# Performance work log

Measured on AMD Instinct MI355X. Metric: run time of the kernel, lower is better.

The kernel has to match this reference:

```python
import jax, jax.numpy as jnp
import numpy as np
from jax import lax

B, CIN, COUT, H, W = 4, 256, 256, 64, 64
KH = KW = 3
STRIDE = PAD = DIL = 1
GROUPS = 1
K = KH * KW
HO = (H + 2 * PAD - DIL * (KH - 1) - 1) // STRIDE + 1
WO = (W + 2 * PAD - DIL * (KW - 1) - 1) // STRIDE + 1
DN = ('NCHW', 'OIHW', 'NCHW')


def _sep_conv(x, dw, pw):
    # Separable2d: depthwise kxk conv (stride/pad/dilation) then pointwise 1x1.
    y = lax.conv_general_dilated(x, dw, (STRIDE, STRIDE), [(PAD, PAD), (PAD, PAD)],
                                 rhs_dilation=(DIL, DIL), feature_group_count=x.shape[1],
                                 dimension_numbers=DN)
    return lax.conv_general_dilated(y, pw, (1, 1), 'VALID', dimension_numbers=DN)


def _deform_conv2d(x, offset, mask, weight, bias):
    Bb, Cin, Hh, Ww = x.shape
    O = weight.shape[0]
    G = offset.shape[1] // (2 * K)  # offset groups
    offs = offset.reshape(Bb, G, K, 2, HO, WO)
    dy, dx = offs[:, :, :, 0], offs[:, :, :, 1]  # [B,G,K,Ho,Wo]
    ki, kj = jnp.meshgrid(jnp.arange(KH), jnp.arange(KW), indexing='ij')
    base_y = (-PAD + ki.reshape(K, 1) * DIL + jnp.arange(HO)[None, :] * STRIDE).astype(x.dtype)  # [K,Ho]
    base_x = (-PAD + kj.reshape(K, 1) * DIL + jnp.arange(WO)[None, :] * STRIDE).astype(x.dtype)  # [K,Wo]
    py = base_y[None, None, :, :, None] + dy  # [B,G,K,Ho,Wo]
    px = base_x[None, None, :, None, :] + dx

    xg = x.reshape(Bb, G, Cin // G, Hh, Ww)

    def bilinear(img, py, px):
        # img [C,H,W], py/px [K,Ho,Wo]; zero-padding outside bounds.
        y0 = jnp.floor(py)
        x0 = jnp.floor(px)
        out = jnp.zeros((img.shape[0],) + py.shape, img.dtype)
        for a, (iy, wy) in enumerate((((y0), (y0 + 1 - py)), ((y0 + 1), (py - y0)))):
            for b, (ix, wx) in enumerate((((x0), (x0 + 1 - px)), ((x0 + 1), (px - x0)))):
                valid = (iy >= 0) & (iy < Hh) & (ix >= 0) & (ix < Ww)
                iyc = jnp.clip(iy, 0, Hh - 1).astype(jnp.int32)
                ixc = jnp.clip(ix, 0, Ww - 1).astype(jnp.int32)
                v = img[:, iyc, ixc]  # [C,K,Ho,Wo]
                out = out + v * (wy * wx * valid)[None]
        return out

    sampled = jax.vmap(jax.vmap(bilinear))(xg, py, px)  # [B,G,C/G,K,Ho,Wo]
    m = mask.reshape(Bb, G, K, HO, WO)
    sampled = sampled * m[:, :, None]

    cols = sampled.reshape(Bb, Cin, K, HO, WO).reshape(Bb, GROUPS, Cin // GROUPS, K, HO, WO)
    wr = weight.reshape(GROUPS, O // GROUPS, Cin // GROUPS, K)
    out = jnp.einsum('bgckhw,gock->bgohw', cols, wr).reshape(Bb, O, HO, WO)
    return out + bias[None, :, None, None]


def setup_inputs() -> dict:
    key = jax.random.key(0)
    ks = jax.random.split(key, 7)
    x = jax.random.normal(ks[0], (B, CIN, H, W), jnp.float32)
    weight = jax.random.normal(ks[1], (COUT, CIN // GROUPS, KH, KW), jnp.float32) / np.sqrt(CIN * K)
    bias = jax.random.normal(ks[2], (COUT,), jnp.float32) * 0.01
    off_dw = jax.random.normal(ks[3], (CIN, 1, KH, KW), jnp.float32) * 0.01
    off_pw = jax.random.normal(ks[4], (2 * K * GROUPS, CIN, 1, 1), jnp.float32) * 0.01
    mask_dw = jax.random.normal(ks[5], (CIN, 1, KH, KW), jnp.float32) * 0.01
    mask_pw = jax.random.normal(ks[6], (K * GROUPS, CIN, 1, 1), jnp.float32) * 0.01
    return dict(x=x, weight=weight, bias=bias, off_dw=off_dw, off_pw=off_pw,
                mask_dw=mask_dw, mask_pw=mask_pw)


def reference(x, weight, bias, off_dw, off_pw, mask_dw, mask_pw):
    offset = _sep_conv(x, off_dw, off_pw)                       # [B,2*K,Ho,Wo]
    mask = jax.nn.sigmoid(_sep_conv(x, mask_dw, mask_pw)) * 2.0  # MaskSigmoid(scale=2)
    return _deform_conv2d(x, offset, mask, weight, bias)
```

## Files before the change

### kernel.cpp

```cpp
#include <hip/hip_runtime.h>

#define CIN   256
#define COUT  256
#define HH    64
#define WW    64
#define KD    2304
#define NPIX  16384
#define SPLIT 16
#define CPS   (CIN / SPLIT)
#define NSTEP 18

typedef __attribute__((ext_vector_type(4))) float  float4v;
typedef __attribute__((ext_vector_type(4))) unsigned int uint4v;
typedef _Float16 h2 __attribute__((ext_vector_type(2)));
typedef _Float16 h8 __attribute__((ext_vector_type(8)));
typedef unsigned int u32;
typedef unsigned short u16;

__device__ __forceinline__ h2 as_h2(u32 v) { union { u32 u; h2 h; } x; x.u = v; return x.h; }
__device__ __forceinline__ u32 as_u32(h2 h) { union { u32 u; h2 h; } x; x.h = h; return x.u; }
__device__ __forceinline__ u16 f2h_bits(float f) { _Float16 h = (_Float16)f; return *(u16*)&h; }
__device__ __forceinline__ u32 packh2(float a, float b) {
  h2 h; h[0] = (_Float16)a; h[1] = (_Float16)b; return as_u32(h);
}

__device__ __forceinline__ void gload_lds16(const void* g, void* l) {
  __builtin_amdgcn_global_load_lds((const __attribute__((address_space(1))) u32*)g,
                                   (__attribute__((address_space(3))) u32*)l, 16, 0, 0);
}

__global__ __launch_bounds__(256) void offmask_part_kernel(
    const float* __restrict__ x,
    const float* __restrict__ off_dw, const float* __restrict__ off_pw,
    const float* __restrict__ mask_dw, const float* __restrict__ mask_pw,
    u32* __restrict__ part2, u16* __restrict__ xt)
{
  int m = blockIdx.x * 256 + threadIdx.x;
  int s = blockIdx.y;
  int b = m >> 12, pix = m & 4095;
  int ho = pix >> 6, wo = pix & 63;
  const float* xb = x + (size_t)b * CIN * 4096;

  float acc[27];
#pragma unroll
  for (int j = 0; j < 27; ++j) acc[j] = 0.f;
  u16 ctr[16];

  int c0 = s * CPS;
  for (int ci = 0; ci < CPS; ++ci) {
    int c = c0 + ci;
    const float* xc = xb + (size_t)c * 4096;
    float d_off = 0.f, d_msk = 0.f;
#pragma unroll
    for (int t = 0; t < 9; ++t) {
      int gy = ho + t / 3 - 1, gx = wo + t % 3 - 1;
      bool ok = (gy >= 0) & (gy < HH) & (gx >= 0) & (gx < WW);
      float v = ok ? xc[gy * 64 + gx] : 0.f;
      if (t == 4) ctr[ci] = f2h_bits(v);
      d_off += v * off_dw[c * 9 + t];
      d_msk += v * mask_dw[c * 9 + t];
    }
#pragma unroll
    for (int j = 0; j < 18; ++j) acc[j] += d_off * off_pw[j * 256 + c];
#pragma unroll
    for (int j = 0; j < 9; ++j) acc[18 + j] += d_msk * mask_pw[j * 256 + c];
  }
  *(uint4v*)(xt + (size_t)m * 256 + c0)     = *(uint4v*)&ctr[0];
  *(uint4v*)(xt + (size_t)m * 256 + c0 + 8) = *(uint4v*)&ctr[8];

  uint4v o[4];
#pragma unroll
  for (int k = 0; k < 13; ++k) o[k >> 2][k & 3] = packh2(acc[2 * k], acc[2 * k + 1]);
  o[3][1] = packh2(acc[26], 0.f);
  o[3][2] = 0; o[3][3] = 0;
  uint4v* pp = (uint4v*)(part2 + ((size_t)s * NPIX + m) * 16);
#pragma unroll
  for (int q = 0; q < 4; ++q) pp[q] = o[q];
}

__global__ __launch_bounds__(256) void offmask_reduce_kernel(
    const u32* __restrict__ part2, float* __restrict__ rec)
{
  int i = blockIdx.x * 256 + threadIdx.x;
  int m = i >> 4, k = i & 15;
  int j0 = 2 * k, j1 = 2 * k + 1;
  if (j0 >= 27) { rec[(size_t)m * 32 + j0] = 0.f; rec[(size_t)m * 32 + j1] = 0.f; return; }
  float s0 = 0.f, s1 = 0.f;
#pragma unroll
  for (int s = 0; s < SPLIT; ++s) {
    h2 v = as_h2(part2[((size_t)s * NPIX + m) * 16 + k]);
    s0 += (float)v[0]; s1 += (float)v[1];
  }
  rec[(size_t)m * 32 + j0] = (j0 < 18) ? s0 : 2.f / (1.f + __expf(-s0));
  rec[(size_t)m * 32 + j1] = (j1 < 18) ? s1 : ((j1 < 27) ? 2.f / (1.f + __expf(-s1)) : 0.f);
}

__global__ __launch_bounds__(256) void wconv_kernel(const float* __restrict__ w,
                                                    u16* __restrict__ wb)
{
  int i = blockIdx.x * 256 + threadIdx.x;
  int co = i / KD, rem = i - co * KD;
  int c = rem / 9, kk = rem - c * 9;
  wb[co * KD + kk * 256 + c] = f2h_bits(w[i]);
}

__global__ __launch_bounds__(512, 2) void gemm_fused_kernel(
    const u16* __restrict__ A,
    const u16* __restrict__ xt,
    const float* __restrict__ rec,
    u16* __restrict__ tmp4)
{
  __shared__ __align__(16) u16 lA[3][256 * 32];
  __shared__ __align__(16) u16 lB[2][256 * 32];
  const int tid = threadIdx.x;
  const int ord = blockIdx.x;
  const int xcd = ord & 7, slot = ord >> 3;
  const int ptile = (slot >> 2) * 8 + xcd;
  const int h     = slot & 3;
  const int m0  = ptile * 256;
  const int b_img = ptile >> 4;
  const int cbase = h * 64;
  const int wave = tid >> 6, lane = tid & 63;
  const int wm = wave >> 1, wn = wave & 1;
  const int rl = lane & 15, kq = lane >> 4;
  const int sA = (kq ^ (rl & 3) ^ ((rl >> 2) & 3)) * 8;

  const int rA  = tid >> 2;
  const int koA = ((tid & 3) ^ (rA & 3) ^ ((rA >> 2) & 3)) * 8;
  const u16* aRow0 = A + (size_t)rA * KD + koA;
  const u16* aRow1 = A + (size_t)(rA + 128) * KD + koA;

  const int px_t = tid >> 1;
  const int chh  = (tid & 1) * 16;
  const int m_px = m0 + px_t;
  const int ho = (m_px & 4095) >> 6, wo = m_px & 63;
  const float* rp = rec + (size_t)m_px * 32;
  const u16* xb = xt + (size_t)b_img * 4096 * 256;
  const int swzp = (px_t & 3) ^ ((px_t >> 2) & 3);
  const int wAddr0 = px_t * 32 + ((((tid & 1) * 2)     ^ swzp) * 8);
  const int wAddr1 = px_t * 32 + ((((tid & 1) * 2 + 1) ^ swzp) * 8);

  u32 cOff[4];
  h2  wh[4];

#define KCOL(t_) (((t_) >> 1) * 256 + cbase + ((t_) & 1) * 32)

#define CALC_CORNERS(kk_) do {                                             \
    float dy = rp[(kk_) * 2], dx = rp[(kk_) * 2 + 1], msk = rp[18 + (kk_)];\
    float py  = (float)(ho - 1 + ((kk_) / 3)) + dy;                        \
    float pxf = (float)(wo - 1 + ((kk_) % 3)) + dx;                        \
    float fy = floorf(py), fx = floorf(pxf);                               \
    int y0 = (int)fy, x0 = (int)fx;                                        \
    float wy1 = py - fy, wy0 = 1.f - wy1;                                  \
    float wx1 = pxf - fx, wx0 = 1.f - wx1;                                 \
    _Pragma("unroll")                                                      \
    for (int cr = 0; cr < 4; ++cr) {                                       \
      int iy = y0 + (cr >> 1), ix = x0 + (cr & 1);                         \
      bool valid = (iy >= 0) & (iy < HH) & (ix >= 0) & (ix < WW);          \
      int iyc = min(max(iy, 0), HH - 1), ixc = min(max(ix, 0), WW - 1);    \
      cOff[cr] = (u32)(iyc * 64 + ixc) * 256;                              \
      float wy = (cr >> 1) ? wy1 : wy0;                                    \
      float wx = (cr & 1) ? wx1 : wx0;                                     \
      float wf = valid ? (wy * wx * msk) : 0.f;                            \
      _Float16 hw = (_Float16)wf;                                          \
      wh[cr] = (h2){hw, hw};                                               \
    }                                                                      \
  } while (0)

#define STAGE_A(k_, slot_) do {                                            \
    int k0_ = KCOL(k_);                                                    \
    gload_lds16(aRow0 + k0_, lA[slot_] + tid * 8);                         \
    gload_lds16(aRow1 + k0_, lA[slot_] + (tid + 512) * 8);                 \
  } while (0)

#define SAMP_LOAD(t_, va, vb) do {                                         \
    int c0n_ = cbase + ((t_) & 1) * 32 + chh;                              \
    _Pragma("unroll")                                                      \
    for (int cr = 0; cr < 4; ++cr) {                                       \
      va[cr] = *(const uint4v*)(xb + cOff[cr] + c0n_);                     \
      vb[cr] = *(const uint4v*)(xb + cOff[cr] + c0n_ + 8);                 \
    }                                                                      \
  } while (0)

#define BLEND_WRITE(bufi_, va, vb) do {                                    \
    uint4v o0, o1;                                                         \
    _Pragma("unroll")                                                      \
    for (int w_ = 0; w_ < 4; ++w_) {                                       \
      h2 s0_ = wh[0] * as_h2(va[0][w_]) + wh[1] * as_h2(va[1][w_]);        \
      s0_   += wh[2] * as_h2(va[2][w_]) + wh[3] * as_h2(va[3][w_]);        \
      h2 s1_ = wh[0] * as_h2(vb[0][w_]) + wh[1] * as_h2(vb[1][w_]);        \
      s1_   += wh[2] * as_h2(vb[2][w_]) + wh[3] * as_h2(vb[3][w_]);        \
      o0[w_] = as_u32(s0_); o1[w_] = as_u32(s1_);                          \
    }                                                                      \
    *(uint4v*)&lB[bufi_][wAddr0] = o0;                                     \
    *(uint4v*)&lB[bufi_][wAddr1] = o1;                                     \
  } while (0)

  float4v acc[4][8];
#pragma unroll
  for (int m = 0; m < 4; ++m)
#pragma unroll
    for (int n = 0; n < 8; ++n) acc[m][n] = float4v{0.f, 0.f, 0.f, 0.f};

  {
    CALC_CORNERS(0);
    uint4v va[4], vb[4];
    SAMP_LOAD(0, va, vb);
    STAGE_A(0, 0);
    STAGE_A(1, 1);
    asm volatile("s_waitcnt vmcnt(2)" ::: "memory");
    BLEND_WRITE(0, va, vb);
    asm volatile("s_waitcnt lgkmcnt(0)" ::: "memory");
    __builtin_amdgcn_s_barrier();
  }

  for (int it = 0; it < 3; ++it) {
#pragma unroll
    for (int u = 0; u < 6; ++u) {
      const int t = it * 6 + u;
      const int tn  = (t + 1 == NSTEP) ? 0 : t + 1;
      const int tn2 = (t + 2 >= NSTEP) ? (t + 2 - NSTEP) : t + 2;
      if ((tn & 1) == 0) CALC_CORNERS(tn >> 1);
      uint4v va[4], vb[4];
      SAMP_LOAD(tn, va, vb);
      STAGE_A(tn2, (u + 2) % 3);
      h8 af[4], bf[8];
#pragma unroll
      for (int m = 0; m < 4; ++m)
        af[m] = *(const h8*)&lA[u % 3][(wm * 64 + m * 16 + rl) * 32 + sA];
#pragma unroll
      for (int n = 0; n < 8; ++n)
        bf[n] = *(const h8*)&lB[u & 1][(wn * 128 + n * 16 + rl) * 32 + sA];
#pragma unroll
      for (int m = 0; m < 4; ++m)
#pragma unroll
        for (int n = 0; n < 8; ++n)
          acc[m][n] = __builtin_amdgcn_mfma_f32_16x16x32_f16(af[m], bf[n], acc[m][n], 0, 0, 0);
      asm volatile("s_waitcnt vmcnt(2)" ::: "memory");
      BLEND_WRITE((u + 1) & 1, va, vb);
      asm volatile("s_waitcnt lgkmcnt(0)" ::: "memory");
      __builtin_amdgcn_s_barrier();
    }
  }
#undef STAGE_A
#undef CALC_CORNERS
#undef SAMP_LOAD
#undef BLEND_WRITE
#undef KCOL

  const int p_base = (m0 & 4095) + wn * 128;
  u16* db = tmp4 + (size_t)h * COUT * NPIX + (size_t)b_img * COUT * 4096;
#pragma unroll
  for (int m = 0; m < 4; ++m) {
#pragma unroll
    for (int j = 0; j < 4; ++j) {
      int co = wm * 64 + m * 16 + kq * 4 + j;
#pragma unroll
      for (int n = 0; n < 8; ++n) {
        int pp = p_base + n * 16 + rl;
        db[(size_t)co * 4096 + pp] = f2h_bits(acc[m][n][j]);
      }
    }
  }
}

__global__ __launch_bounds__(256) void add_kernel(const u16* __restrict__ tmp4,
                                                  const float* __restrict__ bias,
                                                  float* __restrict__ out)
{
  size_t i = ((size_t)blockIdx.x * 256 + threadIdx.x) * 8;
  int co = (int)((i >> 12) & 255);
  float bv = bias[co];
  uint4v v0 = *(const uint4v*)(tmp4 + i);
  uint4v v1 = *(const uint4v*)(tmp4 + (size_t)COUT * NPIX + i);
  uint4v v2 = *(const uint4v*)(tmp4 + (size_t)2 * COUT * NPIX + i);
  uint4v v3 = *(const uint4v*)(tmp4 + (size_t)3 * COUT * NPIX + i);
  float4v oA, oB;
#pragma unroll
  for (int w = 0; w < 4; ++w) {
    h2 a = as_h2(v0[w]), b = as_h2(v1[w]), c = as_h2(v2[w]), d = as_h2(v3[w]);
    float lo = (float)a[0] + (float)b[0] + (float)c[0] + (float)d[0] + bv;
    float hi = (float)a[1] + (float)b[1] + (float)c[1] + (float)d[1] + bv;
    if (w < 2) { oA[w * 2] = lo; oA[w * 2 + 1] = hi; }
    else       { oB[(w - 2) * 2] = lo; oB[(w - 2) * 2 + 1] = hi; }
  }
  *(float4v*)(out + i) = oA;
  *(float4v*)(out + i + 4) = oB;
}

extern "C" void kernel_launch(void* const* d_in, const int* in_sizes, int n_in,
                              void* d_out, int out_size, void* d_ws, size_t ws_size,
                              hipStream_t stream) {
  const float* x       = (const float*)d_in[0];
  const float* weight  = (const float*)d_in[1];
  const float* bias    = (const float*)d_in[2];
  const float* off_dw  = (const float*)d_in[3];
  const float* off_pw  = (const float*)d_in[4];
  const float* mask_dw = (const float*)d_in[5];
  const float* mask_pw = (const float*)d_in[6];

  if (ws_size < 45219840ull) return;
  float* rec   = (float*)d_ws;
  u16*   wb    = (u16*)((char*)d_ws + 2097152);
  u16*   xt    = (u16*)((char*)d_ws + 3276800);
  u32*   part2 = (u32*)((char*)d_ws + 11665408);
  u16*   tmp4  = (u16*)((char*)d_ws + 11665408);
  float* out   = (float*)d_out;

  wconv_kernel<<<dim3(2304), dim3(256), 0, stream>>>(weight, wb);
  offmask_part_kernel<<<dim3(NPIX / 256, SPLIT), dim3(256), 0, stream>>>(
      x, off_dw, off_pw, mask_dw, mask_pw, part2, xt);
  offmask_reduce_kernel<<<dim3(NPIX * 16 / 256), dim3(256), 0, stream>>>(part2, rec);
  gemm_fused_kernel<<<dim3(256), dim3(512), 0, stream>>>(wb, xt, rec, tmp4);
  add_kernel<<<dim3(COUT * NPIX / 8 / 256), dim3(256), 0, stream>>>(tmp4, bias, out);
}
```

Measured before the change: 93.79 us.

## Drop split-K in fused deform GEMM, keep sampled B in registers, fuse bias epilogue

The GEMM no longer splits the channel dimension four ways across blocks. Each block now owns 64 pixels across the full K=2304 and all 256 output channels, so the fp16 partial buffer and the separate add kernel go away and bias is added in the epilogue. Each wave samples its own 16 pixels straight into the MFMA B-operand registers, which removes the LDS B buffer and its write/barrier traffic. In exchange the weight matrix is streamed through LDS once per 64-pixel tile instead of once per 256-pixel tile (four times more A traffic). The launch also drops to 256-thread blocks with 72 smaller K steps, which means more barriers and less MFMA work per step.

```diff
diff --git a/kernel.cpp b/kernel.cpp
--- a/kernel.cpp
+++ b/kernel.cpp
@@ -8,7 +8,7 @@
 #define NPIX  16384
 #define SPLIT 16
 #define CPS   (CIN / SPLIT)
-#define NSTEP 18
+#define NSTEP 72
 
 typedef __attribute__((ext_vector_type(4))) float  float4v;
 typedef __attribute__((ext_vector_type(4))) unsigned int uint4v;
@@ -104,46 +104,38 @@
   wb[co * KD + kk * 256 + c] = f2h_bits(w[i]);
 }
 
-__global__ __launch_bounds__(512, 2) void gemm_fused_kernel(
+__global__ __launch_bounds__(256) void gemm_fused_kernel(
     const u16* __restrict__ A,
     const u16* __restrict__ xt,
     const float* __restrict__ rec,
-    u16* __restrict__ tmp4)
+    const float* __restrict__ bias,
+    float* __restrict__ out)
 {
   __shared__ __align__(16) u16 lA[3][256 * 32];
-  __shared__ __align__(16) u16 lB[2][256 * 32];
   const int tid = threadIdx.x;
-  const int ord = blockIdx.x;
-  const int xcd = ord & 7, slot = ord >> 3;
-  const int ptile = (slot >> 2) * 8 + xcd;
-  const int h     = slot & 3;
-  const int m0  = ptile * 256;
-  const int b_img = ptile >> 4;
-  const int cbase = h * 64;
+  const int ptile = blockIdx.x;
+  const int m0 = ptile * 64;
+  const int b_img = ptile >> 6;
   const int wave = tid >> 6, lane = tid & 63;
-  const int wm = wave >> 1, wn = wave & 1;
   const int rl = lane & 15, kq = lane >> 4;
   const int sA = (kq ^ (rl & 3) ^ ((rl >> 2) & 3)) * 8;
 
   const int rA  = tid >> 2;
   const int koA = ((tid & 3) ^ (rA & 3) ^ ((rA >> 2) & 3)) * 8;
-  const u16* aRow0 = A + (size_t)rA * KD + koA;
-  const u16* aRow1 = A + (size_t)(rA + 128) * KD + koA;
-
-  const int px_t = tid >> 1;
-  const int chh  = (tid & 1) * 16;
-  const int m_px = m0 + px_t;
+  const u16* aRow[4];
+#pragma unroll
+  for (int q = 0; q < 4; ++q) aRow[q] = A + (size_t)(rA + q * 64) * KD + koA;
+
+  const int m_px = m0 + wave * 16 + rl;
   const int ho = (m_px & 4095) >> 6, wo = m_px & 63;
   const float* rp = rec + (size_t)m_px * 32;
   const u16* xb = xt + (size_t)b_img * 4096 * 256;
-  const int swzp = (px_t & 3) ^ ((px_t >> 2) & 3);
-  const int wAddr0 = px_t * 32 + ((((tid & 1) * 2)     ^ swzp) * 8);
-  const int wAddr1 = px_t * 32 + ((((tid & 1) * 2 + 1) ^ swzp) * 8);
 
   u32 cOff[4];
   h2  wh[4];
-
-#define KCOL(t_) (((t_) >> 1) * 256 + cbase + ((t_) & 1) * 32)
+  uint4v sv[4];
+
+#define KCOL(t_) (((t_) >> 3) * 256 + ((t_) & 7) * 32)
 
 #define CALC_CORNERS(kk_) do {                                             \
     float dy = rp[(kk_) * 2], dx = rp[(kk_) * 2 + 1], msk = rp[18 + (kk_)];\
@@ -167,125 +159,86 @@
     }                                                                      \
   } while (0)
 
-#define STAGE_A(k_, slot_) do {                                            \
+#define STAGE_A(k_, sl_) do {                                              \
     int k0_ = KCOL(k_);                                                    \
-    gload_lds16(aRow0 + k0_, lA[slot_] + tid * 8);                         \
-    gload_lds16(aRow1 + k0_, lA[slot_] + (tid + 512) * 8);                 \
-  } while (0)
-
-#define SAMP_LOAD(t_, va, vb) do {                                         \
-    int c0n_ = cbase + ((t_) & 1) * 32 + chh;                              \
-    _Pragma("unroll")                                                      \
-    for (int cr = 0; cr < 4; ++cr) {                                       \
-      va[cr] = *(const uint4v*)(xb + cOff[cr] + c0n_);                     \
-      vb[cr] = *(const uint4v*)(xb + cOff[cr] + c0n_ + 8);                 \
+    _Pragma("unroll")                                                      \
+    for (int q = 0; q < 4; ++q)                                            \
+      gload_lds16(aRow[q] + k0_, lA[sl_] + q * 2048 + tid * 8);            \
+  } while (0)
+
+#define SAMP(t_) do {                                                      \
+    int c0_ = ((t_) & 7) * 32 + kq * 8;                                    \
+    _Pragma("unroll")                                                      \
+    for (int cr = 0; cr < 4; ++cr)                                         \
+      sv[cr] = *(const uint4v*)(xb + cOff[cr] + c0_);                      \
+  } while (0)
+
+#define BLEND(bf_) do {                                                    \
+    _Pragma("unroll")                                                      \
+    for (int w_ = 0; w_ < 4; ++w_) {                                       \
+      h2 s_ = wh[0] * as_h2(sv[0][w_]) + wh[1] * as_h2(sv[1][w_]);         \
+      s_   += wh[2] * as_h2(sv[2][w_]) + wh[3] * as_h2(sv[3][w_]);         \
+      ((u32*)&(bf_))[w_] = as_u32(s_);                                     \
     }                                                                      \
   } while (0)
 
-#define BLEND_WRITE(bufi_, va, vb) do {                                    \
-    uint4v o0, o1;                                                         \
-    _Pragma("unroll")                                                      \
-    for (int w_ = 0; w_ < 4; ++w_) {                                       \
-      h2 s0_ = wh[0] * as_h2(va[0][w_]) + wh[1] * as_h2(va[1][w_]);        \
-      s0_   += wh[2] * as_h2(va[2][w_]) + wh[3] * as_h2(va[3][w_]);        \
-      h2 s1_ = wh[0] * as_h2(vb[0][w_]) + wh[1] * as_h2(vb[1][w_]);        \
-      s1_   += wh[2] * as_h2(vb[2][w_]) + wh[3] * as_h2(vb[3][w_]);        \
-      o0[w_] = as_u32(s0_); o1[w_] = as_u32(s1_);                          \
-    }                                                                      \
-    *(uint4v*)&lB[bufi_][wAddr0] = o0;                                     \
-    *(uint4v*)&lB[bufi_][wAddr1] = o1;                                     \
-  } while (0)
-
-  float4v acc[4][8];
-#pragma unroll
-  for (int m = 0; m < 4; ++m)
-#pragma unroll
-    for (int n = 0; n < 8; ++n) acc[m][n] = float4v{0.f, 0.f, 0.f, 0.f};
+  float4v acc[16];
+#pragma unroll
+  for (int m = 0; m < 16; ++m) acc[m] = float4v{0.f, 0.f, 0.f, 0.f};
 
   {
     CALC_CORNERS(0);
-    uint4v va[4], vb[4];
-    SAMP_LOAD(0, va, vb);
+    SAMP(0);
     STAGE_A(0, 0);
     STAGE_A(1, 1);
-    asm volatile("s_waitcnt vmcnt(2)" ::: "memory");
-    BLEND_WRITE(0, va, vb);
+    asm volatile("s_waitcnt vmcnt(4)" ::: "memory");
+    __builtin_amdgcn_s_barrier();
+  }
+
+  int sl = 0;
+  for (int t = 0; t < NSTEP; ++t) {
+    h8 bf;
+    BLEND(bf);
+    const int tn = (t + 1 == NSTEP) ? 0 : t + 1;
+    if ((tn & 7) == 0) CALC_CORNERS(tn >> 3);
+    SAMP(tn);
+    const int tn2 = (t + 2 >= NSTEP) ? (t + 2 - NSTEP) : t + 2;
+    const int sl2 = (sl >= 1) ? sl - 1 : 2;
+    STAGE_A(tn2, sl2);
+    const u16* laP = lA[0] + sl * (256 * 32);
+#pragma unroll
+    for (int half = 0; half < 2; ++half) {
+      h8 af[8];
+#pragma unroll
+      for (int m = 0; m < 8; ++m)
+        af[m] = *(const h8*)&laP[(half * 128 + m * 16 + rl) * 32 + sA];
+#pragma unroll
+      for (int m = 0; m < 8; ++m)
+        acc[half * 8 + m] =
+            __builtin_amdgcn_mfma_f32_16x16x32_f16(af[m], bf, acc[half * 8 + m], 0, 0, 0);
+    }
+    asm volatile("s_waitcnt vmcnt(4)" ::: "memory");
     asm volatile("s_waitcnt lgkmcnt(0)" ::: "memory");
     __builtin_amdgcn_s_barrier();
-  }
-
-  for (int it = 0; it < 3; ++it) {
-#pragma unroll
-    for (int u = 0; u < 6; ++u) {
-      const int t = it * 6 + u;
-      const int tn  = (t + 1 == NSTEP) ? 0 : t + 1;
-      const int tn2 = (t + 2 >= NSTEP) ? (t + 2 - NSTEP) : t + 2;
-      if ((tn & 1) == 0) CALC_CORNERS(tn >> 1);
-      uint4v va[4], vb[4];
-      SAMP_LOAD(tn, va, vb);
-      STAGE_A(tn2, (u + 2) % 3);
-      h8 af[4], bf[8];
-#pragma unroll
-      for (int m = 0; m < 4; ++m)
-        af[m] = *(const h8*)&lA[u % 3][(wm * 64 + m * 16 + rl) * 32 + sA];
-#pragma unroll
-      for (int n = 0; n < 8; ++n)
-        bf[n] = *(const h8*)&lB[u & 1][(wn * 128 + n * 16 + rl) * 32 + sA];
-#pragma unroll
-      for (int m = 0; m < 4; ++m)
-#pragma unroll
-        for (int n = 0; n < 8; ++n)
-          acc[m][n] = __builtin_amdgcn_mfma_f32_16x16x32_f16(af[m], bf[n], acc[m][n], 0, 0, 0);
-      asm volatile("s_waitcnt vmcnt(2)" ::: "memory");
-      BLEND_WRITE((u + 1) & 1, va, vb);
-      asm volatile("s_waitcnt lgkmcnt(0)" ::: "memory");
-      __builtin_amdgcn_s_barrier();
-    }
+    sl = (sl == 2) ? 0 : sl + 1;
   }
 #undef STAGE_A
 #undef CALC_CORNERS
-#undef SAMP_LOAD
-#undef BLEND_WRITE
+#undef SAMP
+#undef BLEND
 #undef KCOL
 
-  const int p_base = (m0 & 4095) + wn * 128;
-  u16* db = tmp4 + (size_t)h * COUT * NPIX + (size_t)b_img * COUT * 4096;
-#pragma unroll
-  for (int m = 0; m < 4; ++m) {
+  float* ob = out + (size_t)b_img * COUT * 4096;
+  const int px = (m0 & 4095) + wave * 16 + rl;
+#pragma unroll
+  for (int m = 0; m < 16; ++m) {
+    int co_base = (m >> 3) * 128 + (m & 7) * 16 + kq * 4;
 #pragma unroll
     for (int j = 0; j < 4; ++j) {
-      int co = wm * 64 + m * 16 + kq * 4 + j;
-#pragma unroll
-      for (int n = 0; n < 8; ++n) {
-        int pp = p_base + n * 16 + rl;
-        db[(size_t)co * 4096 + pp] = f2h_bits(acc[m][n][j]);
-      }
+      int co = co_base + j;
+      ob[(size_t)co * 4096 + px] = acc[m][j] + bias[co];
     }
   }
-}
-
-__global__ __launch_bounds__(256) void add_kernel(const u16* __restrict__ tmp4,
-                                                  const float* __restrict__ bias,
-                                                  float* __restrict__ out)
-{
-  size_t i = ((size_t)blockIdx.x * 256 + threadIdx.x) * 8;
-  int co = (int)((i >> 12) & 255);
-  float bv = bias[co];
-  uint4v v0 = *(const uint4v*)(tmp4 + i);
-  uint4v v1 = *(const uint4v*)(tmp4 + (size_t)COUT * NPIX + i);
-  uint4v v2 = *(const uint4v*)(tmp4 + (size_t)2 * COUT * NPIX + i);
-  uint4v v3 = *(const uint4v*)(tmp4 + (size_t)3 * COUT * NPIX + i);
-  float4v oA, oB;
-#pragma unroll
-  for (int w = 0; w < 4; ++w) {
-    h2 a = as_h2(v0[w]), b = as_h2(v1[w]), c = as_h2(v2[w]), d = as_h2(v3[w]);
-    float lo = (float)a[0] + (float)b[0] + (float)c[0] + (float)d[0] + bv;
-    float hi = (float)a[1] + (float)b[1] + (float)c[1] + (float)d[1] + bv;
-    if (w < 2) { oA[w * 2] = lo; oA[w * 2 + 1] = hi; }
-    else       { oB[(w - 2) * 2] = lo; oB[(w - 2) * 2 + 1] = hi; }
-  }
-  *(float4v*)(out + i) = oA;
-  *(float4v*)(out + i + 4) = oB;
 }
 
 extern "C" void kernel_launch(void* const* d_in, const int* in_sizes, int n_in,
@@ -299,18 +252,16 @@
   const float* mask_dw = (const float*)d_in[5];
   const float* mask_pw = (const float*)d_in[6];
 
-  if (ws_size < 45219840ull) return;
+  if (ws_size < 28442624ull) return;
   float* rec   = (float*)d_ws;
   u16*   wb    = (u16*)((char*)d_ws + 2097152);
   u16*   xt    = (u16*)((char*)d_ws + 3276800);
   u32*   part2 = (u32*)((char*)d_ws + 11665408);
-  u16*   tmp4  = (u16*)((char*)d_ws + 11665408);
   float* out   = (float*)d_out;
 
   wconv_kernel<<<dim3(2304), dim3(256), 0, stream>>>(weight, wb);
   offmask_part_kernel<<<dim3(NPIX / 256, SPLIT), dim3(256), 0, stream>>>(
       x, off_dw, off_pw, mask_dw, mask_pw, part2, xt);
   offmask_reduce_kernel<<<dim3(NPIX * 16 / 256), dim3(256), 0, stream>>>(part2, rec);
-  gemm_fused_kernel<<<dim3(256), dim3(512), 0, stream>>>(wb, xt, rec, tmp4);
-  add_kernel<<<dim3(COUT * NPIX / 8 / 256), dim3(256), 0, stream>>>(tmp4, bias, out);
-}
+  gemm_fused_kernel<<<dim3(256), dim3(256), 0, stream>>>(wb, xt, rec, bias, out);
+}
```

Measured after the change: 98.70 us. +5.2%, slower.
